# Kernel tuning notes

Measured on AMD Instinct MI355X. Metric: run time of the kernel, lower is better.

The kernel has to match this reference:

```python
import jax, jax.numpy as jnp
import numpy as np

V = 100000          # vocab size
D = 256             # hidden dim
B, N = 32, 128      # batch, max_len
K = 100             # noise_ratio
NORM_TERM = 11.512925  # log(V), norm_term='auto'
BACKOFF_PROB = 1e-10


def setup_inputs() -> dict:
    key = jax.random.key(0)
    ks = jax.random.split(key, 6)
    target = jax.random.randint(ks[0], (B, N), 0, V)
    noise_samples = jax.random.randint(ks[1], (B, N, K), 0, V)
    hidden = jax.random.normal(ks[2], (B, N, D), dtype=jnp.float32) * 0.1
    weight = jax.random.normal(ks[3], (V, D), dtype=jnp.float32) * 0.05
    bias = jax.random.normal(ks[4], (V,), dtype=jnp.float32) * 0.01
    u = jax.random.uniform(ks[5], (V,), dtype=jnp.float32) + BACKOFF_PROB
    noise_probs = u / jnp.sum(u)  # normalized noise distribution
    return {"target": target, "noise_samples": noise_samples, "hidden": hidden,
            "weight": weight, "bias": bias, "noise_probs": noise_probs}


def reference(target, noise_samples, hidden, weight, bias, noise_probs):
    # score_noise = log P_noise(noise_samples)   (B,N,K) -- irregular gather on (V,)
    score_noise = jnp.log(noise_probs)[noise_samples]
    # get_score (IndexLinear): gathered output-embedding dot products
    w_t = weight[target]                                   # (B,N,D)
    score_model = jnp.einsum('bnd,bnd->bn', hidden, w_t) + bias[target] - NORM_TERM
    w_n = weight[noise_samples]                            # (B,N,K,D) big gather
    score_noise_in_model = (jnp.einsum('bnd,bnkd->bnk', hidden, w_n)
                            + bias[noise_samples] - NORM_TERM)
    # NCE binary classification loss (score_target_in_noise passed as zeros)
    log_k = jnp.log(jnp.float32(K))
    logit_true = score_model - log_k                        # (B,N) label=1
    logit_noise = score_noise_in_model - score_noise - log_k  # (B,N,K) label=0
    # BCE-with-logits: -log sigmoid(x) = softplus(-x); -log(1-sigmoid(x)) = softplus(x)
    loss = jax.nn.softplus(-logit_true) + jnp.sum(jax.nn.softplus(logit_noise), axis=-1)
    # reduction='elementwise_mean'
    return jnp.mean(loss)
```

## Files before the change

### kernel.cpp

```cpp
#include <hip/hip_runtime.h>
#include <math.h>

#define V 100000
#define D 256
#define B 32
#define N 128
#define K 100
#define NPOS (B * N)
#define NPAIR (NPOS * (K + 1))
#define BIN_ROWS 32
#define NBIN (V / BIN_ROWS)
#define NSHARD 16
#define CAP_S 32
#define MAXTOT (NSHARD * CAP_S)
#define SLAB_W (D + 8)
#define NORM_TERM 11.512925f
#define LOG_K 4.605170186f

typedef float f32x4 __attribute__((ext_vector_type(4)));
typedef unsigned short u16;

__device__ __forceinline__ float softplus(float x) {
    return fmaxf(x, 0.f) + __logf(1.f + __expf(-fabsf(x)));
}
__device__ __forceinline__ unsigned f32_to_bf16_bits(float x) {
    unsigned u = __float_as_uint(x);
    u += 0x7FFFu + ((u >> 16) & 1u);
    return u >> 16;
}

template <int CTRL>
__device__ __forceinline__ float dpp_add(float x) {
    int y = __builtin_amdgcn_update_dpp(__float_as_int(x), __float_as_int(x),
                                        CTRL, 0xF, 0xF, false);
    return x + __int_as_float(y);
}
__device__ __forceinline__ float quarter_sum(float x) {
    x = dpp_add<0xB1>(x);
    x = dpp_add<0x4E>(x);
    x = dpp_add<0x141>(x);
    x = dpp_add<0x140>(x);
    return x;
}

__global__ __launch_bounds__(256) void scatter_kernel(
    const int* __restrict__ target, const int* __restrict__ noise,
    int* __restrict__ cursor, unsigned* __restrict__ buf)
{
    const int p = blockIdx.x * 256 + threadIdx.x;
    if (p >= NPAIR) return;
    int row, pos; unsigned flag;
    if (p < NPOS * K) { pos = p / K; row = noise[p]; flag = 0u; }
    else              { pos = p - NPOS * K; row = target[pos]; flag = 1u; }
    const int bin   = row >> 5;
    const int shard = blockIdx.x & (NSHARD - 1);
    const int cell  = bin * NSHARD + shard;
    const int slot  = atomicAdd(&cursor[cell], 1);
    if (slot < CAP_S)
        buf[(size_t)cell * CAP_S + slot] =
            ((unsigned)(row & (BIN_ROWS - 1)) << 13) | ((unsigned)pos << 1) | flag;
}

__global__ __launch_bounds__(256, 6) void compute_kernel(
    const float* __restrict__ hidden, const float* __restrict__ weight,
    const float* __restrict__ bias, const float* __restrict__ noise_probs,
    const int* __restrict__ cursor, const unsigned* __restrict__ buf,
    float* __restrict__ out)
{
    __shared__ u16      slab[BIN_ROWS * SLAB_W];
    __shared__ float    sbias[BIN_ROWS];
    __shared__ float    slogp[BIN_ROWS];
    __shared__ unsigned plist[MAXTOT];
    __shared__ int      scnt[NSHARD];
    __shared__ int      pref[NSHARD + 1];
    __shared__ float    wsum[4];

    const int bin = blockIdx.x;
    const int tid = threadIdx.x;

    if (tid < NSHARD)
        scnt[tid] = min(cursor[bin * NSHARD + tid], CAP_S);
    __syncthreads();
    if (tid == 0) {
        int s = 0;
        #pragma unroll
        for (int i = 0; i < NSHARD; ++i) { pref[i] = s; s += scnt[i]; }
        pref[NSHARD] = s;
    }
    __syncthreads();
    const int total = pref[NSHARD];
    if (total == 0) return;

    const int wave = tid >> 6;
    const int lane = tid & 63;
    const int q    = lane >> 4;
    const int ql   = lane & 15;
    const int row0 = bin * BIN_ROWS;

    for (int r = wave; r < BIN_ROWS; r += 4) {
        const f32x4 w4 = __builtin_nontemporal_load(
            (const f32x4*)(weight + (size_t)(row0 + r) * D + lane * 4));
        uint2 b;
        b.x = f32_to_bf16_bits(w4.x) | (f32_to_bf16_bits(w4.y) << 16);
        b.y = f32_to_bf16_bits(w4.z) | (f32_to_bf16_bits(w4.w) << 16);
        *(uint2*)(slab + r * SLAB_W + lane * 4) = b;
    }
    if (tid < BIN_ROWS) {
        sbias[tid] = bias[row0 + tid];
        slogp[tid] = __logf(noise_probs[row0 + tid]);
    }
    for (int i = tid; i < total; i += 256) {
        int s = 0;
        #pragma unroll
        for (int j = 1; j < NSHARD; ++j) s += (i >= pref[j]);
        plist[i] = buf[((size_t)(bin * NSHARD + s)) * CAP_S + (i - pref[s])];
    }
    __syncthreads();

    const int p0 = wave * 4 + q;

    unsigned rec_c  = (p0      < total) ? plist[p0]      : 0u;
    unsigned rec_nx = (p0 + 16 < total) ? plist[p0 + 16] : 0u;

    f32x4 hc[4], hn[4];
    uint2 wc[4], wn[4];

    {
        const float* hp = hidden + (size_t)((rec_c >> 1) & (NPOS - 1)) * D + ql * 4;
        const u16*   wp = slab + ((rec_c >> 13) & (BIN_ROWS - 1)) * SLAB_W + ql * 4;
        #pragma unroll
        for (int i = 0; i < 4; ++i) {
            hc[i] = *(const f32x4*)(hp + i * 64);
            wc[i] = *(const uint2*)(wp + i * 64);
        }
        const float* hp2 = hidden + (size_t)((rec_nx >> 1) & (NPOS - 1)) * D + ql * 4;
        const u16*   wp2 = slab + ((rec_nx >> 13) & (BIN_ROWS - 1)) * SLAB_W + ql * 4;
        #pragma unroll
        for (int i = 0; i < 4; ++i) {
            hn[i] = *(const f32x4*)(hp2 + i * 64);
            wn[i] = *(const uint2*)(wp2 + i * 64);
        }
    }

    float loss = 0.f;
    for (int base = wave * 4; base < total; base += 16) {
        const int p = base + q;
        const unsigned rec_2 = (p + 32 < total) ? plist[p + 32] : 0u;

        float s0 = 0.f, s1 = 0.f, s2 = 0.f, s3 = 0.f;
        s0 = fmaf(__uint_as_float(wc[0].x << 16),         hc[0].x, s0);
        s0 = fmaf(__uint_as_float(wc[0].x & 0xffff0000u), hc[0].y, s0);
        s0 = fmaf(__uint_as_float(wc[0].y << 16),         hc[0].z, s0);
        s0 = fmaf(__uint_as_float(wc[0].y & 0xffff0000u), hc[0].w, s0);
        s1 = fmaf(__uint_as_float(wc[1].x << 16),         hc[1].x, s1);
        s1 = fmaf(__uint_as_float(wc[1].x & 0xffff0000u), hc[1].y, s1);
        s1 = fmaf(__uint_as_float(wc[1].y << 16),         hc[1].z, s1);
        s1 = fmaf(__uint_as_float(wc[1].y & 0xffff0000u), hc[1].w, s1);
        s2 = fmaf(__uint_as_float(wc[2].x << 16),         hc[2].x, s2);
        s2 = fmaf(__uint_as_float(wc[2].x & 0xffff0000u), hc[2].y, s2);
        s2 = fmaf(__uint_as_float(wc[2].y << 16),         hc[2].z, s2);
        s2 = fmaf(__uint_as_float(wc[2].y & 0xffff0000u), hc[2].w, s2);
        s3 = fmaf(__uint_as_float(wc[3].x << 16),         hc[3].x, s3);
        s3 = fmaf(__uint_as_float(wc[3].x & 0xffff0000u), hc[3].y, s3);
        s3 = fmaf(__uint_as_float(wc[3].y << 16),         hc[3].z, s3);
        s3 = fmaf(__uint_as_float(wc[3].y & 0xffff0000u), hc[3].w, s3);

        const float r = quarter_sum((s0 + s1) + (s2 + s3));

        const int rloc = (int)((rec_c >> 13) & (BIN_ROWS - 1));
        const float score = r + sbias[rloc] - NORM_TERM;
        const float x = (rec_c & 1u) ? (LOG_K - score)
                                     : (score - slogp[rloc] - LOG_K);
        if ((p < total) && ql == 0) loss += softplus(x);

        rec_c  = rec_nx;
        rec_nx = rec_2;
        #pragma unroll
        for (int i = 0; i < 4; ++i) { hc[i] = hn[i]; wc[i] = wn[i]; }
        const float* hp = hidden + (size_t)((rec_nx >> 1) & (NPOS - 1)) * D + ql * 4;
        const u16*   wp = slab + ((rec_nx >> 13) & (BIN_ROWS - 1)) * SLAB_W + ql * 4;
        #pragma unroll
        for (int i = 0; i < 4; ++i) {
            hn[i] = *(const f32x4*)(hp + i * 64);
            wn[i] = *(const uint2*)(wp + i * 64);
        }
    }

    loss += __shfl_xor(loss, 16, 64);
    loss += __shfl_xor(loss, 32, 64);
    if (lane == 0) wsum[wave] = loss;
    __syncthreads();
    if (tid == 0)
        atomicAdd(out, (wsum[0] + wsum[1] + wsum[2] + wsum[3])
                       * (1.0f / (float)NPOS));
}

extern "C" void kernel_launch(void* const* d_in, const int* in_sizes, int n_in,
                              void* d_out, int out_size, void* d_ws, size_t ws_size,
                              hipStream_t stream) {
    const int*   target      = (const int*)d_in[0];
    const int*   noise       = (const int*)d_in[1];
    const float* hidden      = (const float*)d_in[2];
    const float* weight      = (const float*)d_in[3];
    const float* bias        = (const float*)d_in[4];
    const float* noise_probs = (const float*)d_in[5];
    float* out = (float*)d_out;

    int*      cursor = (int*)d_ws;
    unsigned* buf    = (unsigned*)((char*)d_ws + (size_t)NBIN * NSHARD * 4);

    hipMemsetAsync(cursor, 0, (size_t)NBIN * NSHARD * 4, stream);
    hipMemsetAsync(out, 0, sizeof(float), stream);

    scatter_kernel<<<(NPAIR + 255) / 256, 256, 0, stream>>>(
        target, noise, cursor, buf);
    compute_kernel<<<NBIN, 256, 0, stream>>>(
        hidden, weight, bias, noise_probs, cursor, buf, out);
}
```

Baseline: 223.7 us.

## Pre-convert weight table to bf16 in scatter kernel and read bf16 in compute

The scatter kernel now handles two pairs per thread and, when workspace allows, converts the whole fp32 weight table into a bf16 copy. The compute kernel loads its row slab from this bf16 table instead of converting fp32 rows itself, and occupancy bounds are raised. This halves the bytes the compute kernel reads but adds a full extra read and write pass over the table every call, raising total memory traffic.

```diff
diff --git a/kernel.cpp b/kernel.cpp
--- a/kernel.cpp
+++ b/kernel.cpp
@@ -8,17 +8,22 @@
 #define K 100
 #define NPOS (B * N)
 #define NPAIR (NPOS * (K + 1))
+#define NPAIR2 (NPAIR / 2)
+#define SCATTER_BLOCKS (NPAIR2 / 256)
 #define BIN_ROWS 32
 #define NBIN (V / BIN_ROWS)
 #define NSHARD 16
 #define CAP_S 32
 #define MAXTOT (NSHARD * CAP_S)
 #define SLAB_W (D + 8)
+#define CVT_VEC (V * D / 4)
 #define NORM_TERM 11.512925f
 #define LOG_K 4.605170186f
 
-typedef float f32x4 __attribute__((ext_vector_type(4)));
+typedef float    f32x4 __attribute__((ext_vector_type(4)));
+typedef unsigned u32x2 __attribute__((ext_vector_type(2)));
 typedef unsigned short u16;
+typedef u16      u16x4 __attribute__((ext_vector_type(4)));
 
 __device__ __forceinline__ float softplus(float x) {
     return fmaxf(x, 0.f) + __logf(1.f + __expf(-fabsf(x)));
@@ -43,28 +48,49 @@
     return x;
 }
 
-__global__ __launch_bounds__(256) void scatter_kernel(
+__global__ __launch_bounds__(256) void scatter_convert_kernel(
     const int* __restrict__ target, const int* __restrict__ noise,
-    int* __restrict__ cursor, unsigned* __restrict__ buf)
+    const float* __restrict__ weight,
+    int* __restrict__ cursor, unsigned* __restrict__ buf,
+    u16* __restrict__ wtab, int do_convert)
 {
-    const int p = blockIdx.x * 256 + threadIdx.x;
-    if (p >= NPAIR) return;
-    int row, pos; unsigned flag;
-    if (p < NPOS * K) { pos = p / K; row = noise[p]; flag = 0u; }
-    else              { pos = p - NPOS * K; row = target[pos]; flag = 1u; }
-    const int bin   = row >> 5;
-    const int shard = blockIdx.x & (NSHARD - 1);
-    const int cell  = bin * NSHARD + shard;
-    const int slot  = atomicAdd(&cursor[cell], 1);
-    if (slot < CAP_S)
-        buf[(size_t)cell * CAP_S + slot] =
-            ((unsigned)(row & (BIN_ROWS - 1)) << 13) | ((unsigned)pos << 1) | flag;
-}
-
-__global__ __launch_bounds__(256, 6) void compute_kernel(
+    const int t = blockIdx.x * 256 + threadIdx.x;
+
+    int cell[2]; unsigned rec[2];
+    #pragma unroll
+    for (int i = 0; i < 2; ++i) {
+        const int pp = t + i * NPAIR2;
+        int row, pos; unsigned flag;
+        if (pp < NPOS * K) { pos = pp / K; row = noise[pp]; flag = 0u; }
+        else               { pos = pp - NPOS * K; row = target[pos]; flag = 1u; }
+        cell[i] = (row >> 5) * NSHARD + ((blockIdx.x * 2 + i) & (NSHARD - 1));
+        rec[i]  = ((unsigned)(row & (BIN_ROWS - 1)) << 13)
+                | ((unsigned)pos << 1) | flag;
+    }
+    const int s0 = atomicAdd(&cursor[cell[0]], 1);
+    const int s1 = atomicAdd(&cursor[cell[1]], 1);
+    if (s0 < CAP_S) buf[(size_t)cell[0] * CAP_S + s0] = rec[0];
+    if (s1 < CAP_S) buf[(size_t)cell[1] * CAP_S + s1] = rec[1];
+
+    if (do_convert) {
+        const int nthreads = SCATTER_BLOCKS * 256;
+        for (int i = t; i < CVT_VEC; i += nthreads) {
+            const f32x4 w4 = __builtin_nontemporal_load((const f32x4*)weight + i);
+            u16x4 b;
+            b.x = (u16)f32_to_bf16_bits(w4.x);
+            b.y = (u16)f32_to_bf16_bits(w4.y);
+            b.z = (u16)f32_to_bf16_bits(w4.z);
+            b.w = (u16)f32_to_bf16_bits(w4.w);
+            *((u16x4*)wtab + i) = b;
+        }
+    }
+}
+
+__global__ __launch_bounds__(256, 8) void compute_kernel(
     const float* __restrict__ hidden, const float* __restrict__ weight,
     const float* __restrict__ bias, const float* __restrict__ noise_probs,
     const int* __restrict__ cursor, const unsigned* __restrict__ buf,
+    const u16* __restrict__ wtab, int use_bf16,
     float* __restrict__ out)
 {
     __shared__ u16      slab[BIN_ROWS * SLAB_W];
@@ -97,13 +123,21 @@
     const int ql   = lane & 15;
     const int row0 = bin * BIN_ROWS;
 
-    for (int r = wave; r < BIN_ROWS; r += 4) {
-        const f32x4 w4 = __builtin_nontemporal_load(
-            (const f32x4*)(weight + (size_t)(row0 + r) * D + lane * 4));
-        uint2 b;
-        b.x = f32_to_bf16_bits(w4.x) | (f32_to_bf16_bits(w4.y) << 16);
-        b.y = f32_to_bf16_bits(w4.z) | (f32_to_bf16_bits(w4.w) << 16);
-        *(uint2*)(slab + r * SLAB_W + lane * 4) = b;
+    if (use_bf16) {
+        for (int r = wave; r < BIN_ROWS; r += 4) {
+            const u32x2 b = __builtin_nontemporal_load(
+                (const u32x2*)(wtab + (size_t)(row0 + r) * D + lane * 4));
+            *(u32x2*)(slab + r * SLAB_W + lane * 4) = b;
+        }
+    } else {
+        for (int r = wave; r < BIN_ROWS; r += 4) {
+            const f32x4 w4 = __builtin_nontemporal_load(
+                (const f32x4*)(weight + (size_t)(row0 + r) * D + lane * 4));
+            u32x2 b;
+            b.x = f32_to_bf16_bits(w4.x) | (f32_to_bf16_bits(w4.y) << 16);
+            b.y = f32_to_bf16_bits(w4.z) | (f32_to_bf16_bits(w4.w) << 16);
+            *(u32x2*)(slab + r * SLAB_W + lane * 4) = b;
+        }
     }
     if (tid < BIN_ROWS) {
         sbias[tid] = bias[row0 + tid];
@@ -123,7 +157,7 @@
     unsigned rec_nx = (p0 + 16 < total) ? plist[p0 + 16] : 0u;
 
     f32x4 hc[4], hn[4];
-    uint2 wc[4], wn[4];
+    u32x2 wc[4], wn[4];
 
     {
         const float* hp = hidden + (size_t)((rec_c >> 1) & (NPOS - 1)) * D + ql * 4;
@@ -131,14 +165,14 @@
         #pragma unroll
         for (int i = 0; i < 4; ++i) {
             hc[i] = *(const f32x4*)(hp + i * 64);
-            wc[i] = *(const uint2*)(wp + i * 64);
+            wc[i] = *(const u32x2*)(wp + i * 64);
         }
         const float* hp2 = hidden + (size_t)((rec_nx >> 1) & (NPOS - 1)) * D + ql * 4;
         const u16*   wp2 = slab + ((rec_nx >> 13) & (BIN_ROWS - 1)) * SLAB_W + ql * 4;
         #pragma unroll
         for (int i = 0; i < 4; ++i) {
             hn[i] = *(const f32x4*)(hp2 + i * 64);
-            wn[i] = *(const uint2*)(wp2 + i * 64);
+            wn[i] = *(const u32x2*)(wp2 + i * 64);
         }
     }
 
@@ -182,7 +216,7 @@
         #pragma unroll
         for (int i = 0; i < 4; ++i) {
             hn[i] = *(const f32x4*)(hp + i * 64);
-            wn[i] = *(const uint2*)(wp + i * 64);
+            wn[i] = *(const u32x2*)(wp + i * 64);
         }
     }
 
@@ -206,14 +240,20 @@
     const float* noise_probs = (const float*)d_in[5];
     float* out = (float*)d_out;
 
+    const size_t cursor_bytes = (size_t)NBIN * NSHARD * 4;
+    const size_t buf_bytes    = (size_t)NBIN * NSHARD * CAP_S * 4;
+    const size_t wtab_bytes   = (size_t)V * D * 2;
     int*      cursor = (int*)d_ws;
-    unsigned* buf    = (unsigned*)((char*)d_ws + (size_t)NBIN * NSHARD * 4);
-
-    hipMemsetAsync(cursor, 0, (size_t)NBIN * NSHARD * 4, stream);
-    hipMemsetAsync(out, 0, sizeof(float), stream);
-
-    scatter_kernel<<<(NPAIR + 255) / 256, 256, 0, stream>>>(
-        target, noise, cursor, buf);
+    unsigned* buf    = (unsigned*)((char*)d_ws + cursor_bytes);
+    u16*      wtab   = (u16*)((char*)d_ws + cursor_bytes + buf_bytes);
+    const int use_bf16 =
+        (ws_size >= cursor_bytes + buf_bytes + wtab_bytes) ? 1 : 0;
+
+    (void)hipMemsetAsync(cursor, 0, cursor_bytes, stream);
+    (void)hipMemsetAsync(out, 0, sizeof(float), stream);
+
+    scatter_convert_kernel<<<SCATTER_BLOCKS, 256, 0, stream>>>(
+        target, noise, weight, cursor, buf, wtab, use_bf16);
     compute_kernel<<<NBIN, 256, 0, stream>>>(
-        hidden, weight, bias, noise_probs, cursor, buf, out);
-}
+        hidden, weight, bias, noise_probs, cursor, buf, wtab, use_bf16, out);
+}
```

New measurement: 247.2 us. 10.5% more time.
